# Performance work log

Measured on AMD Instinct MI355X. Metric: run time of the kernel, lower is better.

The kernel has to match this reference:

```python
import jax, jax.numpy as jnp
import numpy as np

N = 50000
E = 400000
D_IN = 128
D_OUT = 128
D_NODE = 6
EPS = 1e-5


def _layernorm(h, g, b):
    mu = jnp.mean(h, axis=-1, keepdims=True)
    var = jnp.var(h, axis=-1, keepdims=True)
    return (h - mu) * jax.lax.rsqrt(var + EPS) * g + b


def setup_inputs() -> dict:
    key = jax.random.key(0)
    ks = jax.random.split(key, 8)
    d_cat = 3 * D_IN + 2 * D_NODE  # 396 = input_dim*3 + 12
    return {
        "x": jax.random.normal(ks[0], (N, D_NODE), jnp.float32),
        "edge_index": jax.random.randint(ks[1], (2, E), 0, N, dtype=jnp.int32),
        "edge_attr": jax.random.normal(ks[2], (E, D_IN), jnp.float32),
        "mask": (jax.random.uniform(ks[3], (E,)) > 0.5).astype(jnp.float32),
        "num_nodes": N,
        "W_edge": jax.random.normal(ks[4], (d_cat, D_OUT), jnp.float32) / np.sqrt(d_cat).astype(np.float32),
        "b_edge": jnp.zeros((D_OUT,), jnp.float32),
        "W1": jax.random.normal(ks[5], (D_OUT, 2 * D_OUT), jnp.float32) / np.sqrt(D_OUT).astype(np.float32),
        "b1": jnp.zeros((2 * D_OUT,), jnp.float32),
        "W2": jax.random.normal(ks[6], (2 * D_OUT, D_OUT), jnp.float32) / np.sqrt(2 * D_OUT).astype(np.float32),
        "b2": jnp.zeros((D_OUT,), jnp.float32),
        "g1": jnp.ones((D_OUT,), jnp.float32),
        "be1": jnp.zeros((D_OUT,), jnp.float32),
        "g2": jnp.ones((D_OUT,), jnp.float32),
        "be2": jnp.zeros((D_OUT,), jnp.float32),
    }


def reference(x, edge_attr, mask, W_edge, b_edge, W1, b1, W2, b2, g1, be1, g2, be2, edge_index, num_nodes):
    row, col = edge_index[0], edge_index[1]
    # mean-like aggregation of incoming edge features onto destination nodes
    agg = jax.ops.segment_sum(edge_attr * mask[:, None], col, num_segments=num_nodes)  # [N, D_IN]
    den = jax.ops.segment_sum(mask, col, num_segments=num_nodes) + 1.0  # [N]
    node_rep = jnp.concatenate([agg / den[:, None], x], axis=1)  # [N, D_IN + D_NODE]
    edge_rep = jnp.concatenate([node_rep[row], node_rep[col], edge_attr], axis=-1)  # [E, 3*D_IN+12]
    h = _layernorm(edge_attr[:, :D_OUT] + edge_rep @ W_edge + b_edge, g1, be1)  # [E, D_OUT]
    out = _layernorm(h + jax.nn.relu(h @ W1 + b1) @ W2 + b2, g2, be2)  # [E, D_OUT]
    return (node_rep, out)
```

## Files before the change

kernel.cpp:

```cpp
#include <hip/hip_runtime.h>


constexpr int NN = 50000;
constexpr int NE = 400000;
constexpr int DI = 128;
constexpr int DN = 6;
constexpr int DR = 134;
constexpr float LN_EPS = 1e-5f;

using f4 = __attribute__((ext_vector_type(4))) float;
using s8 = __attribute__((ext_vector_type(8))) short;

__device__ __forceinline__ unsigned short f2bf(float f) {
    unsigned u = __float_as_uint(f);
    u += 0x7fff + ((u >> 16) & 1);
    return (unsigned short)(u >> 16);
}

__device__ __forceinline__ float bf2f(unsigned short b) {
    return __uint_as_float((unsigned)b << 16);
}

__device__ __forceinline__ float red16(float v) {
    int x;
    x = __builtin_amdgcn_update_dpp(0, __float_as_int(v), 0x121, 0xf, 0xf, true);
    v += __int_as_float(x);
    x = __builtin_amdgcn_update_dpp(0, __float_as_int(v), 0x122, 0xf, 0xf, true);
    v += __int_as_float(x);
    x = __builtin_amdgcn_update_dpp(0, __float_as_int(v), 0x124, 0xf, 0xf, true);
    v += __int_as_float(x);
    x = __builtin_amdgcn_update_dpp(0, __float_as_int(v), 0x128, 0xf, 0xf, true);
    v += __int_as_float(x);
    return v;
}

__global__ __launch_bounds__(256) void deg_kernel(
    const float* __restrict__ mask, const int* __restrict__ ei,
    int* __restrict__ deg)
{
    int e = blockIdx.x * 256 + threadIdx.x;
    if (e >= NE) return;
    if (mask[e] != 0.f) atomicAdd(&deg[ei[NE + e]], 1);
}

__global__ __launch_bounds__(1024) void scan_kernel(
    const int* __restrict__ deg, int* __restrict__ offs, int* __restrict__ cursor)
{
    __shared__ int part[1024];
    const int t = threadIdx.x;
    constexpr int CH = (NN + 1023) / 1024;
    const int base = t * CH;
    const int lim  = min(base + CH, NN);

    int s = 0;
    for (int i = base; i < lim; ++i) s += deg[i];
    part[t] = s;
    __syncthreads();
    for (int off = 1; off < 1024; off <<= 1) {
        int add = (t >= off) ? part[t - off] : 0;
        __syncthreads();
        part[t] += add;
        __syncthreads();
    }
    int run = (t == 0) ? 0 : part[t - 1];
    for (int i = base; i < lim; ++i) {
        offs[i]   = run;
        cursor[i] = run;
        run += deg[i];
    }
    if (t == 1023) offs[NN] = part[1023];
}

__global__ __launch_bounds__(256) void binfill_kernel(
    const float* __restrict__ mask, const int* __restrict__ ei,
    int* __restrict__ cursor, int* __restrict__ bucket)
{
    int e = blockIdx.x * 256 + threadIdx.x;
    if (e >= NE) return;
    if (mask[e] != 0.f) {
        int pos = atomicAdd(&cursor[ei[NE + e]], 1);
        bucket[pos] = e;
    }
}

__global__ __launch_bounds__(256) void gather_kernel(
    const float* __restrict__ edge_attr, const float* __restrict__ mask,
    const float* __restrict__ x, const int* __restrict__ offs,
    const int* __restrict__ bucket, float* __restrict__ node_out)
{
    int n = blockIdx.x * 4 + (threadIdx.x >> 6);
    if (n >= NN) return;
    const int lane = threadIdx.x & 63;
    const int beg = offs[n], end = offs[n + 1];
    float2 acc = make_float2(0.f, 0.f);
    float den = 0.f;
    for (int j = beg; j < end; ++j) {
        int e = bucket[j];
        float m = mask[e];
        float2 v = *reinterpret_cast<const float2*>(edge_attr + (size_t)e * 128 + lane * 2);
        acc.x += v.x * m;
        acc.y += v.y * m;
        den   += m;
    }
    float inv = 1.f / (den + 1.f);
    float2 o = make_float2(acc.x * inv, acc.y * inv);
    *reinterpret_cast<float2*>(node_out + (size_t)n * DR + lane * 2) = o;
    if (lane < DN) node_out[(size_t)n * DR + DI + lane] = x[n * DN + lane];
}

__global__ __launch_bounds__(256) void prep_w_kernel(
    const float* __restrict__ W_edge, const float* __restrict__ W1,
    const float* __restrict__ W2,
    unsigned short* __restrict__ WcT, unsigned short* __restrict__ W1T,
    unsigned short* __restrict__ W2T)
{
    int idx = blockIdx.x * 256 + threadIdx.x;
    if (idx < 16384) {
        int n = idx >> 7, k = idx & 127;
        float v = W_edge[(268 + k) * 128 + n] + (k == n ? 1.f : 0.f);
        WcT[n * 128 + k] = f2bf(v);
    } else if (idx < 49152) {
        int j = idx - 16384;
        int n = j >> 7, k = j & 127;
        W1T[n * 128 + k] = f2bf(W1[k * 256 + n]);
    } else if (idx < 81920) {
        int j = idx - 49152;
        int n = j >> 8, k = j & 255;
        W2T[n * 256 + k] = f2bf(W2[k * 128 + n]);
    }
}

__global__ __launch_bounds__(256) void pq_kernel(
    const float* __restrict__ nr, const float* __restrict__ W_edge,
    const float* __restrict__ b_edge,
    float* __restrict__ P, float* __restrict__ Q)
{
    __shared__ float As[32 * 136];
    const int t = threadIdx.x;
    const int n0 = blockIdx.x * 32;

    for (int idx = t; idx < 32 * 136; idx += 256) {
        int n = idx / 136, k = idx - n * 136;
        float v = 0.f;
        if (n0 + n < NN && k < DR) v = nr[(size_t)(n0 + n) * DR + k];
        As[idx] = v;
    }
    __syncthreads();

    const int et = t >> 5, jt = t & 31;
    float4 accP[4], accQ[4];
    #pragma unroll
    for (int i = 0; i < 4; ++i) {
        accP[i] = make_float4(0.f, 0.f, 0.f, 0.f);
        accQ[i] = make_float4(0.f, 0.f, 0.f, 0.f);
    }
    for (int k0 = 0; k0 < 136; k0 += 4) {
        float4 wa[4], wb[4];
        #pragma unroll
        for (int d = 0; d < 4; ++d) {
            wa[d] = *reinterpret_cast<const float4*>(&W_edge[(size_t)(k0 + d) * 128 + 4 * jt]);
            wb[d] = *reinterpret_cast<const float4*>(&W_edge[(size_t)(134 + k0 + d) * 128 + 4 * jt]);
        }
        #pragma unroll
        for (int i = 0; i < 4; ++i) {
            float4 a4 = *reinterpret_cast<const float4*>(&As[(4 * et + i) * 136 + k0]);
            accP[i].x += a4.x * wa[0].x + a4.y * wa[1].x + a4.z * wa[2].x + a4.w * wa[3].x;
            accP[i].y += a4.x * wa[0].y + a4.y * wa[1].y + a4.z * wa[2].y + a4.w * wa[3].y;
            accP[i].z += a4.x * wa[0].z + a4.y * wa[1].z + a4.z * wa[2].z + a4.w * wa[3].z;
            accP[i].w += a4.x * wa[0].w + a4.y * wa[1].w + a4.z * wa[2].w + a4.w * wa[3].w;
            accQ[i].x += a4.x * wb[0].x + a4.y * wb[1].x + a4.z * wb[2].x + a4.w * wb[3].x;
            accQ[i].y += a4.x * wb[0].y + a4.y * wb[1].y + a4.z * wb[2].y + a4.w * wb[3].y;
            accQ[i].z += a4.x * wb[0].z + a4.y * wb[1].z + a4.z * wb[2].z + a4.w * wb[3].z;
            accQ[i].w += a4.x * wb[0].w + a4.y * wb[1].w + a4.z * wb[2].w + a4.w * wb[3].w;
        }
    }
    float4 bev = *reinterpret_cast<const float4*>(&b_edge[4 * jt]);
    #pragma unroll
    for (int i = 0; i < 4; ++i) {
        int n = n0 + 4 * et + i;
        if (n < NN) {
            float4 p = accP[i];
            p.x += bev.x; p.y += bev.y; p.z += bev.z; p.w += bev.w;
            *reinterpret_cast<float4*>(&P[(size_t)n * 128 + 4 * jt]) = p;
            *reinterpret_cast<float4*>(&Q[(size_t)n * 128 + 4 * jt]) = accQ[i];
        }
    }
}

constexpr int PA = 136;
constexpr int PU = 264;
constexpr int ET = 64;
constexpr int NTILE = NE / ET;

__global__ __launch_bounds__(1024, 4) void ffn_kernel(
    const float* __restrict__ edge_attr,
    const int* __restrict__ ei,
    const float* __restrict__ P,
    const float* __restrict__ Q,
    const unsigned short* __restrict__ WcT,
    const unsigned short* __restrict__ W1T,
    const unsigned short* __restrict__ W2T,
    const float* __restrict__ b1, const float* __restrict__ b2,
    const float* __restrict__ g1, const float* __restrict__ be1,
    const float* __restrict__ g2, const float* __restrict__ be2,
    float* __restrict__ out)
{
    __shared__ short lds_a[ET * PA];
    __shared__ short lds_u[ET * PU];
    __shared__ float red_part[2][8][32][2];
    __shared__ float musig[2][ET][2];

    const int t    = threadIdx.x;
    const int w    = t >> 6;
    const int lane = t & 63;
    const int q    = lane >> 4;
    const int c    = lane & 15;
    const int mg   = w >> 3;
    const int cw   = w & 7;

    s8 wcf[4], w1f[2][4], w2f[8];
    #pragma unroll
    for (int k0 = 0; k0 < 4; ++k0)
        wcf[k0] = *reinterpret_cast<const s8*>(WcT + (cw * 16 + c) * 128 + k0 * 32 + q * 8);
    #pragma unroll
    for (int nt = 0; nt < 2; ++nt)
        #pragma unroll
        for (int k0 = 0; k0 < 4; ++k0)
            w1f[nt][k0] = *reinterpret_cast<const s8*>(W1T + (cw * 32 + nt * 16 + c) * 128 + k0 * 32 + q * 8);
    #pragma unroll
    for (int k0 = 0; k0 < 8; ++k0)
        w2f[k0] = *reinterpret_cast<const s8*>(W2T + (cw * 16 + c) * 256 + k0 * 32 + q * 8);

    const float g1c  = g1[cw * 16 + c],  be1c = be1[cw * 16 + c];
    const float b1v0 = b1[cw * 32 + c],  b1v1 = b1[cw * 32 + 16 + c];
    const float b2c  = b2[cw * 16 + c];
    const float g2c  = g2[cw * 16 + c],  be2c = be2[cw * 16 + c];

    const int srow = t >> 4;
    const int sti  = t & 15;

    for (int tile = blockIdx.x; tile < NTILE; tile += gridDim.x) {
        const int e0 = tile * ET;

        {
            const float4* src = reinterpret_cast<const float4*>(
                edge_attr + (size_t)(e0 + srow) * 128 + sti * 8);
            float4 v0 = src[0], v1 = src[1];
            s8 bb;
            bb[0] = (short)f2bf(v0.x); bb[1] = (short)f2bf(v0.y);
            bb[2] = (short)f2bf(v0.z); bb[3] = (short)f2bf(v0.w);
            bb[4] = (short)f2bf(v1.x); bb[5] = (short)f2bf(v1.y);
            bb[6] = (short)f2bf(v1.z); bb[7] = (short)f2bf(v1.w);
            *reinterpret_cast<s8*>(&lds_a[srow * PA + sti * 8]) = bb;
        }
        __syncthreads();

        f4 acc1[2];
        acc1[0] = {0.f, 0.f, 0.f, 0.f};
        acc1[1] = {0.f, 0.f, 0.f, 0.f};
        #pragma unroll
        for (int k0 = 0; k0 < 4; ++k0)
            #pragma unroll
            for (int mt = 0; mt < 2; ++mt) {
                s8 a = *reinterpret_cast<const s8*>(&lds_a[(mg * 32 + mt * 16 + c) * PA + k0 * 32 + q * 8]);
                acc1[mt] = __builtin_amdgcn_mfma_f32_16x16x32_bf16(a, wcf[k0], acc1[mt], 0, 0, 0);
            }

        #pragma unroll
        for (int mt = 0; mt < 2; ++mt)
            #pragma unroll
            for (int reg = 0; reg < 4; ++reg) {
                int e  = e0 + mg * 32 + mt * 16 + q * 4 + reg;
                int er = ei[e], ec = ei[NE + e];
                acc1[mt][reg] += P[(size_t)er * 128 + cw * 16 + c]
                               + Q[(size_t)ec * 128 + cw * 16 + c];
            }

        #pragma unroll
        for (int mt = 0; mt < 2; ++mt)
            #pragma unroll
            for (int reg = 0; reg < 4; ++reg) {
                float v  = acc1[mt][reg];
                float sv = red16(v);
                float sq = red16(v * v);
                if (c == 0) {
                    int r = mt * 16 + q * 4 + reg;
                    float2 p2; p2.x = sv; p2.y = sq;
                    *reinterpret_cast<float2*>(&red_part[mg][cw][r][0]) = p2;
                }
            }
        __syncthreads();
        if (t < ET) {
            float s = 0.f, ss = 0.f;
            #pragma unroll
            for (int i = 0; i < 8; ++i) {
                float2 p2 = *reinterpret_cast<const float2*>(&red_part[t >> 5][i][t & 31][0]);
                s += p2.x; ss += p2.y;
            }
            float mu  = s * (1.f / 128.f);
            float var = ss * (1.f / 128.f) - mu * mu;
            float2 m2; m2.x = mu; m2.y = rsqrtf(var + LN_EPS);
            *reinterpret_cast<float2*>(&musig[0][t][0]) = m2;
        }
        __syncthreads();

        #pragma unroll
        for (int mt = 0; mt < 2; ++mt)
            #pragma unroll
            for (int reg = 0; reg < 4; ++reg) {
                int r = mg * 32 + mt * 16 + q * 4 + reg;
                float2 m2 = *reinterpret_cast<const float2*>(&musig[0][r][0]);
                float h = (acc1[mt][reg] - m2.x) * m2.y * g1c + be1c;
                lds_a[r * PA + cw * 16 + c] = (short)f2bf(h);
            }
        __syncthreads();

        f4 acc2[2][2];
        acc2[0][0] = {0.f,0.f,0.f,0.f}; acc2[0][1] = {0.f,0.f,0.f,0.f};
        acc2[1][0] = {0.f,0.f,0.f,0.f}; acc2[1][1] = {0.f,0.f,0.f,0.f};
        #pragma unroll
        for (int k0 = 0; k0 < 4; ++k0)
            #pragma unroll
            for (int mt = 0; mt < 2; ++mt) {
                s8 a = *reinterpret_cast<const s8*>(&lds_a[(mg * 32 + mt * 16 + c) * PA + k0 * 32 + q * 8]);
                acc2[mt][0] = __builtin_amdgcn_mfma_f32_16x16x32_bf16(a, w1f[0][k0], acc2[mt][0], 0, 0, 0);
                acc2[mt][1] = __builtin_amdgcn_mfma_f32_16x16x32_bf16(a, w1f[1][k0], acc2[mt][1], 0, 0, 0);
            }
        #pragma unroll
        for (int mt = 0; mt < 2; ++mt)
            #pragma unroll
            for (int reg = 0; reg < 4; ++reg) {
                int r = mg * 32 + mt * 16 + q * 4 + reg;
                float u0 = fmaxf(acc2[mt][0][reg] + b1v0, 0.f);
                float u1 = fmaxf(acc2[mt][1][reg] + b1v1, 0.f);
                lds_u[r * PU + cw * 32 + c]      = (short)f2bf(u0);
                lds_u[r * PU + cw * 32 + 16 + c] = (short)f2bf(u1);
            }
        __syncthreads();

        f4 acc3[2];
        #pragma unroll
        for (int mt = 0; mt < 2; ++mt)
            #pragma unroll
            for (int reg = 0; reg < 4; ++reg) {
                int r = mg * 32 + mt * 16 + q * 4 + reg;
                acc3[mt][reg] = bf2f((unsigned short)lds_a[r * PA + cw * 16 + c]) + b2c;
            }
        #pragma unroll
        for (int k0 = 0; k0 < 8; ++k0)
            #pragma unroll
            for (int mt = 0; mt < 2; ++mt) {
                s8 a = *reinterpret_cast<const s8*>(&lds_u[(mg * 32 + mt * 16 + c) * PU + k0 * 32 + q * 8]);
                acc3[mt] = __builtin_amdgcn_mfma_f32_16x16x32_bf16(a, w2f[k0], acc3[mt], 0, 0, 0);
            }

        #pragma unroll
        for (int mt = 0; mt < 2; ++mt)
            #pragma unroll
            for (int reg = 0; reg < 4; ++reg) {
                float v  = acc3[mt][reg];
                float sv = red16(v);
                float sq = red16(v * v);
                if (c == 0) {
                    int r = mt * 16 + q * 4 + reg;
                    float2 p2; p2.x = sv; p2.y = sq;
                    *reinterpret_cast<float2*>(&red_part[mg][cw][r][0]) = p2;
                }
            }
        __syncthreads();
        if (t < ET) {
            float s = 0.f, ss = 0.f;
            #pragma unroll
            for (int i = 0; i < 8; ++i) {
                float2 p2 = *reinterpret_cast<const float2*>(&red_part[t >> 5][i][t & 31][0]);
                s += p2.x; ss += p2.y;
            }
            float mu  = s * (1.f / 128.f);
            float var = ss * (1.f / 128.f) - mu * mu;
            float2 m2; m2.x = mu; m2.y = rsqrtf(var + LN_EPS);
            *reinterpret_cast<float2*>(&musig[1][t][0]) = m2;
        }
        __syncthreads();

        #pragma unroll
        for (int mt = 0; mt < 2; ++mt)
            #pragma unroll
            for (int reg = 0; reg < 4; ++reg) {
                int r = mg * 32 + mt * 16 + q * 4 + reg;
                float2 m2 = *reinterpret_cast<const float2*>(&musig[1][r][0]);
                float o = (acc3[mt][reg] - m2.x) * m2.y * g2c + be2c;
                out[(size_t)(e0 + r) * 128 + cw * 16 + c] = o;
            }
    }
}

extern "C" void kernel_launch(void* const* d_in, const int* in_sizes, int n_in,
                              void* d_out, int out_size, void* d_ws, size_t ws_size,
                              hipStream_t stream) {
    const float* x         = (const float*)d_in[0];
    const int*   ei        = (const int*)  d_in[1];
    const float* edge_attr = (const float*)d_in[2];
    const float* mask      = (const float*)d_in[3];
    const float* W_edge    = (const float*)d_in[5];
    const float* b_edge    = (const float*)d_in[6];
    const float* W1        = (const float*)d_in[7];
    const float* b1        = (const float*)d_in[8];
    const float* W2        = (const float*)d_in[9];
    const float* b2        = (const float*)d_in[10];
    const float* g1        = (const float*)d_in[11];
    const float* be1       = (const float*)d_in[12];
    const float* g2        = (const float*)d_in[13];
    const float* be2       = (const float*)d_in[14];

    float* node_out  = (float*)d_out;
    float* out_edges = (float*)d_out + (size_t)NN * DR;

    char* ws = (char*)d_ws;
    int*            deg    = (int*)(ws);
    int*            offs   = (int*)(ws + (256 << 10));
    int*            cursor = (int*)(ws + (512 << 10));
    unsigned short* WcT    = (unsigned short*)(ws + (768 << 10));
    unsigned short* W1T    = (unsigned short*)(ws + (768 << 10) + 32768);
    unsigned short* W2T    = (unsigned short*)(ws + (768 << 10) + 98304);
    int*            bucket = (int*)(ws + (1 << 20));
    float*          P      = (float*)(ws + (1 << 20));
    float*          Q      = (float*)(ws + (1 << 20) + 26214400);

    hipMemsetAsync(deg, 0, (size_t)NN * sizeof(int), stream);

    deg_kernel<<<(NE + 255) / 256, 256, 0, stream>>>(mask, ei, deg);
    scan_kernel<<<1, 1024, 0, stream>>>(deg, offs, cursor);
    binfill_kernel<<<(NE + 255) / 256, 256, 0, stream>>>(mask, ei, cursor, bucket);
    gather_kernel<<<(NN + 3) / 4, 256, 0, stream>>>(edge_attr, mask, x, offs, bucket, node_out);
    prep_w_kernel<<<320, 256, 0, stream>>>(W_edge, W1, W2, WcT, W1T, W2T);
    pq_kernel<<<(NN + 31) / 32, 256, 0, stream>>>(node_out, W_edge, b_edge, P, Q);
    ffn_kernel<<<256, 1024, 0, stream>>>(edge_attr, ei, P, Q, WcT, W1T, W2T,
                                         b1, b2, g1, be1, g2, be2, out_edges);
}
```

Baseline: 866.7 us.

## Swizzle LDS tiles, shrink FFN tile to one row group, shuffle LN stats

The FFN kernel moves from 64-edge tiles on 1024 threads to 32-edge tiles on 512 threads with 512 blocks. Padded LDS rows are replaced by an XOR-swizzled layout to avoid bank conflicts. LayerNorm mean and rstd are now broadcast through wave shuffles instead of a shared musig array, which removes one barrier per LayerNorm. Separately, the gather kernel drops its mask reads because the bucket holds only masked edges, so the degree comes from the offsets; the PQ kernel doubles its node tile to 64 to reuse each weight load across more rows.

```diff
diff --git a/kernel.cpp b/kernel.cpp
--- a/kernel.cpp
+++ b/kernel.cpp
@@ -84,25 +84,22 @@
 }
 
 __global__ __launch_bounds__(256) void gather_kernel(
-    const float* __restrict__ edge_attr, const float* __restrict__ mask,
-    const float* __restrict__ x, const int* __restrict__ offs,
-    const int* __restrict__ bucket, float* __restrict__ node_out)
+    const float* __restrict__ edge_attr, const float* __restrict__ x,
+    const int* __restrict__ offs, const int* __restrict__ bucket,
+    float* __restrict__ node_out)
 {
     int n = blockIdx.x * 4 + (threadIdx.x >> 6);
     if (n >= NN) return;
     const int lane = threadIdx.x & 63;
     const int beg = offs[n], end = offs[n + 1];
     float2 acc = make_float2(0.f, 0.f);
-    float den = 0.f;
     for (int j = beg; j < end; ++j) {
         int e = bucket[j];
-        float m = mask[e];
         float2 v = *reinterpret_cast<const float2*>(edge_attr + (size_t)e * 128 + lane * 2);
-        acc.x += v.x * m;
-        acc.y += v.y * m;
-        den   += m;
-    }
-    float inv = 1.f / (den + 1.f);
+        acc.x += v.x;
+        acc.y += v.y;
+    }
+    float inv = 1.f / (float)(end - beg + 1);
     float2 o = make_float2(acc.x * inv, acc.y * inv);
     *reinterpret_cast<float2*>(node_out + (size_t)n * DR + lane * 2) = o;
     if (lane < DN) node_out[(size_t)n * DR + DI + lane] = x[n * DN + lane];
@@ -135,11 +132,11 @@
     const float* __restrict__ b_edge,
     float* __restrict__ P, float* __restrict__ Q)
 {
-    __shared__ float As[32 * 136];
+    __shared__ float As[64 * 136];
     const int t = threadIdx.x;
-    const int n0 = blockIdx.x * 32;
-
-    for (int idx = t; idx < 32 * 136; idx += 256) {
+    const int n0 = blockIdx.x * 64;
+
+    for (int idx = t; idx < 64 * 136; idx += 256) {
         int n = idx / 136, k = idx - n * 136;
         float v = 0.f;
         if (n0 + n < NN && k < DR) v = nr[(size_t)(n0 + n) * DR + k];
@@ -148,9 +145,9 @@
     __syncthreads();
 
     const int et = t >> 5, jt = t & 31;
-    float4 accP[4], accQ[4];
+    float4 accP[8], accQ[8];
     #pragma unroll
-    for (int i = 0; i < 4; ++i) {
+    for (int i = 0; i < 8; ++i) {
         accP[i] = make_float4(0.f, 0.f, 0.f, 0.f);
         accQ[i] = make_float4(0.f, 0.f, 0.f, 0.f);
     }
@@ -162,8 +159,8 @@
             wb[d] = *reinterpret_cast<const float4*>(&W_edge[(size_t)(134 + k0 + d) * 128 + 4 * jt]);
         }
         #pragma unroll
-        for (int i = 0; i < 4; ++i) {
-            float4 a4 = *reinterpret_cast<const float4*>(&As[(4 * et + i) * 136 + k0]);
+        for (int i = 0; i < 8; ++i) {
+            float4 a4 = *reinterpret_cast<const float4*>(&As[(8 * et + i) * 136 + k0]);
             accP[i].x += a4.x * wa[0].x + a4.y * wa[1].x + a4.z * wa[2].x + a4.w * wa[3].x;
             accP[i].y += a4.x * wa[0].y + a4.y * wa[1].y + a4.z * wa[2].y + a4.w * wa[3].y;
             accP[i].z += a4.x * wa[0].z + a4.y * wa[1].z + a4.z * wa[2].z + a4.w * wa[3].z;
@@ -176,8 +173,8 @@
     }
     float4 bev = *reinterpret_cast<const float4*>(&b_edge[4 * jt]);
     #pragma unroll
-    for (int i = 0; i < 4; ++i) {
-        int n = n0 + 4 * et + i;
+    for (int i = 0; i < 8; ++i) {
+        int n = n0 + 8 * et + i;
         if (n < NN) {
             float4 p = accP[i];
             p.x += bev.x; p.y += bev.y; p.z += bev.z; p.w += bev.w;
@@ -187,12 +184,11 @@
     }
 }
 
-constexpr int PA = 136;
-constexpr int PU = 264;
-constexpr int ET = 64;
+constexpr int ET = 32;
 constexpr int NTILE = NE / ET;
-
-__global__ __launch_bounds__(1024, 4) void ffn_kernel(
+constexpr int FFN_GRID = 512;
+
+__global__ __launch_bounds__(512, 4) void ffn_kernel(
     const float* __restrict__ edge_attr,
     const int* __restrict__ ei,
     const float* __restrict__ P,
@@ -205,18 +201,16 @@
     const float* __restrict__ g2, const float* __restrict__ be2,
     float* __restrict__ out)
 {
-    __shared__ short lds_a[ET * PA];
-    __shared__ short lds_u[ET * PU];
-    __shared__ float red_part[2][8][32][2];
-    __shared__ float musig[2][ET][2];
+    __shared__ short lds_a[ET * 128];
+    __shared__ short lds_u[ET * 256];
+    __shared__ float red_part[8][ET][2];
 
     const int t    = threadIdx.x;
     const int w    = t >> 6;
     const int lane = t & 63;
     const int q    = lane >> 4;
     const int c    = lane & 15;
-    const int mg   = w >> 3;
-    const int cw   = w & 7;
+    const int cw   = w;
 
     s8 wcf[4], w1f[2][4], w2f[8];
     #pragma unroll
@@ -251,7 +245,7 @@
             bb[2] = (short)f2bf(v0.z); bb[3] = (short)f2bf(v0.w);
             bb[4] = (short)f2bf(v1.x); bb[5] = (short)f2bf(v1.y);
             bb[6] = (short)f2bf(v1.z); bb[7] = (short)f2bf(v1.w);
-            *reinterpret_cast<s8*>(&lds_a[srow * PA + sti * 8]) = bb;
+            *reinterpret_cast<s8*>(&lds_a[srow * 128 + (sti ^ (srow & 7)) * 8]) = bb;
         }
         __syncthreads();
 
@@ -262,7 +256,8 @@
         for (int k0 = 0; k0 < 4; ++k0)
             #pragma unroll
             for (int mt = 0; mt < 2; ++mt) {
-                s8 a = *reinterpret_cast<const s8*>(&lds_a[(mg * 32 + mt * 16 + c) * PA + k0 * 32 + q * 8]);
+                s8 a = *reinterpret_cast<const s8*>(
+                    &lds_a[(mt * 16 + c) * 128 + ((k0 * 4 + q) ^ (c & 7)) * 8]);
                 acc1[mt] = __builtin_amdgcn_mfma_f32_16x16x32_bf16(a, wcf[k0], acc1[mt], 0, 0, 0);
             }
 
@@ -270,7 +265,7 @@
         for (int mt = 0; mt < 2; ++mt)
             #pragma unroll
             for (int reg = 0; reg < 4; ++reg) {
-                int e  = e0 + mg * 32 + mt * 16 + q * 4 + reg;
+                int e  = e0 + mt * 16 + q * 4 + reg;
                 int er = ei[e], ec = ei[NE + e];
                 acc1[mt][reg] += P[(size_t)er * 128 + cw * 16 + c]
                                + Q[(size_t)ec * 128 + cw * 16 + c];
@@ -286,32 +281,33 @@
                 if (c == 0) {
                     int r = mt * 16 + q * 4 + reg;
                     float2 p2; p2.x = sv; p2.y = sq;
-                    *reinterpret_cast<float2*>(&red_part[mg][cw][r][0]) = p2;
+                    *reinterpret_cast<float2*>(&red_part[cw][r][0]) = p2;
                 }
             }
         __syncthreads();
-        if (t < ET) {
+
+        float mu_l = 0.f, rs_l = 0.f;
+        if (lane < ET) {
             float s = 0.f, ss = 0.f;
             #pragma unroll
             for (int i = 0; i < 8; ++i) {
-                float2 p2 = *reinterpret_cast<const float2*>(&red_part[t >> 5][i][t & 31][0]);
+                float2 p2 = *reinterpret_cast<const float2*>(&red_part[i][lane][0]);
                 s += p2.x; ss += p2.y;
             }
-            float mu  = s * (1.f / 128.f);
-            float var = ss * (1.f / 128.f) - mu * mu;
-            float2 m2; m2.x = mu; m2.y = rsqrtf(var + LN_EPS);
-            *reinterpret_cast<float2*>(&musig[0][t][0]) = m2;
-        }
-        __syncthreads();
-
-        #pragma unroll
-        for (int mt = 0; mt < 2; ++mt)
-            #pragma unroll
-            for (int reg = 0; reg < 4; ++reg) {
-                int r = mg * 32 + mt * 16 + q * 4 + reg;
-                float2 m2 = *reinterpret_cast<const float2*>(&musig[0][r][0]);
-                float h = (acc1[mt][reg] - m2.x) * m2.y * g1c + be1c;
-                lds_a[r * PA + cw * 16 + c] = (short)f2bf(h);
+            mu_l = s * (1.f / 128.f);
+            float var = ss * (1.f / 128.f) - mu_l * mu_l;
+            rs_l = rsqrtf(var + LN_EPS);
+        }
+
+        #pragma unroll
+        for (int mt = 0; mt < 2; ++mt)
+            #pragma unroll
+            for (int reg = 0; reg < 4; ++reg) {
+                int r = mt * 16 + q * 4 + reg;
+                float mu = __shfl(mu_l, r, 64);
+                float rs = __shfl(rs_l, r, 64);
+                float h = (acc1[mt][reg] - mu) * rs * g1c + be1c;
+                lds_a[r * 128 + ((cw * 2 + (c >> 3)) ^ (r & 7)) * 8 + (c & 7)] = (short)f2bf(h);
             }
         __syncthreads();
 
@@ -322,7 +318,8 @@
         for (int k0 = 0; k0 < 4; ++k0)
             #pragma unroll
             for (int mt = 0; mt < 2; ++mt) {
-                s8 a = *reinterpret_cast<const s8*>(&lds_a[(mg * 32 + mt * 16 + c) * PA + k0 * 32 + q * 8]);
+                s8 a = *reinterpret_cast<const s8*>(
+                    &lds_a[(mt * 16 + c) * 128 + ((k0 * 4 + q) ^ (c & 7)) * 8]);
                 acc2[mt][0] = __builtin_amdgcn_mfma_f32_16x16x32_bf16(a, w1f[0][k0], acc2[mt][0], 0, 0, 0);
                 acc2[mt][1] = __builtin_amdgcn_mfma_f32_16x16x32_bf16(a, w1f[1][k0], acc2[mt][1], 0, 0, 0);
             }
@@ -330,11 +327,13 @@
         for (int mt = 0; mt < 2; ++mt)
             #pragma unroll
             for (int reg = 0; reg < 4; ++reg) {
-                int r = mg * 32 + mt * 16 + q * 4 + reg;
+                int r = mt * 16 + q * 4 + reg;
                 float u0 = fmaxf(acc2[mt][0][reg] + b1v0, 0.f);
                 float u1 = fmaxf(acc2[mt][1][reg] + b1v1, 0.f);
-                lds_u[r * PU + cw * 32 + c]      = (short)f2bf(u0);
-                lds_u[r * PU + cw * 32 + 16 + c] = (short)f2bf(u1);
+                int ch0 = (cw * 4 + (c >> 3)) ^ (r & 7);
+                int ch1 = (cw * 4 + 2 + (c >> 3)) ^ (r & 7);
+                lds_u[r * 256 + ch0 * 8 + (c & 7)] = (short)f2bf(u0);
+                lds_u[r * 256 + ch1 * 8 + (c & 7)] = (short)f2bf(u1);
             }
         __syncthreads();
 
@@ -343,14 +342,16 @@
         for (int mt = 0; mt < 2; ++mt)
             #pragma unroll
             for (int reg = 0; reg < 4; ++reg) {
-                int r = mg * 32 + mt * 16 + q * 4 + reg;
-                acc3[mt][reg] = bf2f((unsigned short)lds_a[r * PA + cw * 16 + c]) + b2c;
+                int r = mt * 16 + q * 4 + reg;
+                acc3[mt][reg] = bf2f((unsigned short)
+                    lds_a[r * 128 + ((cw * 2 + (c >> 3)) ^ (r & 7)) * 8 + (c & 7)]) + b2c;
             }
         #pragma unroll
         for (int k0 = 0; k0 < 8; ++k0)
             #pragma unroll
             for (int mt = 0; mt < 2; ++mt) {
-                s8 a = *reinterpret_cast<const s8*>(&lds_u[(mg * 32 + mt * 16 + c) * PU + k0 * 32 + q * 8]);
+                s8 a = *reinterpret_cast<const s8*>(
+                    &lds_u[(mt * 16 + c) * 256 + ((k0 * 4 + q) ^ (c & 7)) * 8]);
                 acc3[mt] = __builtin_amdgcn_mfma_f32_16x16x32_bf16(a, w2f[k0], acc3[mt], 0, 0, 0);
             }
 
@@ -364,31 +365,32 @@
                 if (c == 0) {
                     int r = mt * 16 + q * 4 + reg;
                     float2 p2; p2.x = sv; p2.y = sq;
-                    *reinterpret_cast<float2*>(&red_part[mg][cw][r][0]) = p2;
+                    *reinterpret_cast<float2*>(&red_part[cw][r][0]) = p2;
                 }
             }
         __syncthreads();
-        if (t < ET) {
+
+        float mu2_l = 0.f, rs2_l = 0.f;
+        if (lane < ET) {
             float s = 0.f, ss = 0.f;
             #pragma unroll
             for (int i = 0; i < 8; ++i) {
-                float2 p2 = *reinterpret_cast<const float2*>(&red_part[t >> 5][i][t & 31][0]);
+                float2 p2 = *reinterpret_cast<const float2*>(&red_part[i][lane][0]);
                 s += p2.x; ss += p2.y;
             }
-            float mu  = s * (1.f / 128.f);
-            float var = ss * (1.f / 128.f) - mu * mu;
-            float2 m2; m2.x = mu; m2.y = rsqrtf(var + LN_EPS);
-            *reinterpret_cast<float2*>(&musig[1][t][0]) = m2;
-        }
-        __syncthreads();
-
-        #pragma unroll
-        for (int mt = 0; mt < 2; ++mt)
-            #pragma unroll
-            for (int reg = 0; reg < 4; ++reg) {
-                int r = mg * 32 + mt * 16 + q * 4 + reg;
-                float2 m2 = *reinterpret_cast<const float2*>(&musig[1][r][0]);
-                float o = (acc3[mt][reg] - m2.x) * m2.y * g2c + be2c;
+            mu2_l = s * (1.f / 128.f);
+            float var = ss * (1.f / 128.f) - mu2_l * mu2_l;
+            rs2_l = rsqrtf(var + LN_EPS);
+        }
+
+        #pragma unroll
+        for (int mt = 0; mt < 2; ++mt)
+            #pragma unroll
+            for (int reg = 0; reg < 4; ++reg) {
+                int r = mt * 16 + q * 4 + reg;
+                float mu = __shfl(mu2_l, r, 64);
+                float rs = __shfl(rs2_l, r, 64);
+                float o = (acc3[mt][reg] - mu) * rs * g2c + be2c;
                 out[(size_t)(e0 + r) * 128 + cw * 16 + c] = o;
             }
     }
@@ -431,9 +433,9 @@
     deg_kernel<<<(NE + 255) / 256, 256, 0, stream>>>(mask, ei, deg);
     scan_kernel<<<1, 1024, 0, stream>>>(deg, offs, cursor);
     binfill_kernel<<<(NE + 255) / 256, 256, 0, stream>>>(mask, ei, cursor, bucket);
-    gather_kernel<<<(NN + 3) / 4, 256, 0, stream>>>(edge_attr, mask, x, offs, bucket, node_out);
+    gather_kernel<<<(NN + 3) / 4, 256, 0, stream>>>(edge_attr, x, offs, bucket, node_out);
     prep_w_kernel<<<320, 256, 0, stream>>>(W_edge, W1, W2, WcT, W1T, W2T);
-    pq_kernel<<<(NN + 31) / 32, 256, 0, stream>>>(node_out, W_edge, b_edge, P, Q);
-    ffn_kernel<<<256, 1024, 0, stream>>>(edge_attr, ei, P, Q, WcT, W1T, W2T,
-                                         b1, b2, g1, be1, g2, be2, out_edges);
-}
+    pq_kernel<<<(NN + 63) / 64, 256, 0, stream>>>(node_out, W_edge, b_edge, P, Q);
+    ffn_kernel<<<FFN_GRID, 512, 0, stream>>>(edge_attr, ei, P, Q, WcT, W1T, W2T,
+                                             b1, b2, g1, be1, g2, be2, out_edges);
+}
```

After: 1.019 ms. 1.18x slower.
